# Kernel tuning notes

Measured on AMD Instinct MI355X. Metric: run time of the kernel, lower is better.

## Reference

```python
import jax, jax.numpy as jnp
import numpy as np

N = 50000          # nodes
K = 16             # neighbors per node
E = N * K          # edges
C_IN = 64
C_OUT = 64
BN_EPS = 1e-5


def _batchnorm(h, gamma, beta):
    # training-mode BatchNorm1d over the edge dimension (biased variance, as torch)
    mean = jnp.mean(h, axis=0)
    var = jnp.mean((h - mean) ** 2, axis=0)
    return gamma * (h - mean) * jax.lax.rsqrt(var + BN_EPS) + beta


def setup_inputs() -> dict:
    key = jax.random.key(0)
    ks = jax.random.split(key, 8)
    x = jax.random.normal(ks[0], (N, C_IN), dtype=jnp.float32)
    # destinations: every node has exactly K incoming edges (avoids empty segments)
    dst = jnp.repeat(jnp.arange(N, dtype=jnp.int64), K)
    src = jax.random.randint(ks[1], (E,), 0, N, dtype=jnp.int64)
    edge_index = jnp.stack([src, dst], axis=0)
    s1 = 1.0 / np.sqrt(2 * C_IN)
    s2 = 1.0 / np.sqrt(C_OUT)
    params = {
        "W1": jax.random.uniform(ks[2], (2 * C_IN, C_OUT), jnp.float32, -s1, s1),
        "b1": jnp.zeros((C_OUT,), jnp.float32),
        "g1": jnp.ones((C_OUT,), jnp.float32),
        "be1": jnp.zeros((C_OUT,), jnp.float32),
        "W2": jax.random.uniform(ks[3], (C_OUT, C_OUT), jnp.float32, -s2, s2),
        "b2": jnp.zeros((C_OUT,), jnp.float32),
        "g2": jnp.ones((C_OUT,), jnp.float32),
        "be2": jnp.zeros((C_OUT,), jnp.float32),
        "W3": jax.random.uniform(ks[4], (C_OUT, C_OUT), jnp.float32, -s2, s2),
        "b3": jnp.zeros((C_OUT,), jnp.float32),
    }
    return {"x": x, "edge_index": edge_index, **params}


def reference(x, edge_index, W1, b1, g1, be1, W2, b2, g2, be2, W3, b3):
    src, dst = edge_index[0], edge_index[1]
    x_i = x[dst]                      # [E, C_in] destination (center) features
    x_j = x[src]                      # [E, C_in] source (neighbor) features
    h = jnp.concatenate([x_i, x_j - x_i], axis=-1)   # [E, 2*C_in]
    h = jax.nn.leaky_relu(_batchnorm(h @ W1 + b1, g1, be1))
    h = jax.nn.leaky_relu(_batchnorm(h @ W2 + b2, g2, be2))
    h = h @ W3 + b3                   # [E, C_out]
    out = jax.ops.segment_max(h, dst, num_segments=N)  # scatter-max per dst node
    res = x                           # identity residual (in_channels == out_channels)
    return jax.nn.leaky_relu(out + res)
```

## Files before the change

### kernel.cpp

```cpp
#include <hip/hip_runtime.h>
#include <hip/hip_fp16.h>

#define N_NODES 50000
#define KNN     16
#define NEDGE   (N_NODES*KNN)
#define NTILE2  (NEDGE/128)
#define NWT     (N_NODES/16)
#define NB2     1024
#define SLOPE   0.01f
#define EPS     1e-5f

typedef __attribute__((ext_vector_type(8))) _Float16 f16x8;
typedef __attribute__((ext_vector_type(4))) float f32x4;

__device__ __forceinline__ unsigned short f2h(float f){
  union{_Float16 h; unsigned short u;} v; v.h = (_Float16)f; return v.u;
}
__device__ __forceinline__ unsigned short h2u(_Float16 h){
  union{_Float16 h; unsigned short u;} v; v.h = h; return v.u;
}
__device__ __forceinline__ f32x4 MFMA(f16x8 a, f16x8 b, f32x4 c){
  return __builtin_amdgcn_mfma_f32_16x16x32_f16(a, b, c, 0, 0, 0);
}
__device__ __forceinline__ float lrelu(float v){ return v>=0.f ? v : SLOPE*v; }

__global__ __launch_bounds__(256) void kInit(const float* __restrict__ W1,
    const float* __restrict__ W2, const float* __restrict__ W3,
    unsigned short* __restrict__ wf)
{
  const int idx = blockIdx.x*256 + threadIdx.x;
  const float* W; int fi; bool fold = false;
  if (idx < 1024)      { W = W1; fi = idx >> 6; fold = (idx < 512); }
  else if (idx < 1536) { W = W2; fi = (idx-1024) >> 6; }
  else                 { W = W3; fi = (idx-1536) >> 6; }
  const int l  = idx & 63;
  const int ks = fi >> 2, nf = fi & 3;
  const int k0 = ks*32 + ((l>>4)<<3);
  const int col = nf*16 + (l&15);
  unsigned short* o = wf + (size_t)idx*8;
#pragma unroll
  for (int e=0;e<8;++e){
    float v = W[(size_t)(k0+e)*64 + col];
    if (fold) v -= W[(size_t)(k0+e+64)*64 + col];
    o[e] = f2h(v);
  }
}

__global__ __launch_bounds__(256) void kUV(const float* __restrict__ x,
    const uint4* __restrict__ wf, unsigned short* __restrict__ Ub,
    unsigned short* __restrict__ Vb)
{
  const int t = threadIdx.x, w = t>>6, l = t&63, lr = l&15, lg = l>>4;
  const int wt = blockIdx.x*4 + w;
  if (wt >= NWT) return;
  f16x8 wfr[16];
#pragma unroll
  for (int f=0;f<16;++f){ union{uint4 v; f16x8 h;}q; q.v = wf[f*64 + l]; wfr[f]=q.h; }
  const int n0 = wt*16;
  const float* xr = x + (size_t)(n0+lr)*64 + lg*8;
  f16x8 a0, a1;
#pragma unroll
  for (int e=0;e<8;++e){ a0[e] = (_Float16)xr[e]; a1[e] = (_Float16)xr[32+e]; }

  f32x4 aU[4], aV[4];
#pragma unroll
  for (int nf=0;nf<4;++nf){
    aU[nf] = (f32x4){0,0,0,0};
    aU[nf] = MFMA(a0, wfr[nf],    aU[nf]);
    aU[nf] = MFMA(a1, wfr[4+nf],  aU[nf]);
    aV[nf] = (f32x4){0,0,0,0};
    aV[nf] = MFMA(a0, wfr[8+nf],  aV[nf]);
    aV[nf] = MFMA(a1, wfr[12+nf], aV[nf]);
  }
#pragma unroll
  for (int nf=0;nf<4;++nf)
#pragma unroll
    for (int r=0;r<4;++r){
      const size_t o = (size_t)(n0 + 4*lg + r)*64 + 16*nf + lr;
      Ub[o] = f2h(aU[nf][r]);
      Vb[o] = f2h(aV[nf][r]);
    }
}

#define LOADUV(U0,U1,V0,V1, nodeId, srcId)                               \
  {                                                                      \
    const unsigned short* Ur = Ub + (size_t)(nodeId)*64 + lg*8;          \
    const unsigned short* Vr = Vb + (size_t)(srcId)*64  + lg*8;          \
    U0 = *(const f16x8*)(Ur); U1 = *(const f16x8*)(Ur + 32);             \
    V0 = *(const f16x8*)(Vr); V1 = *(const f16x8*)(Vr + 32);             \
  }

#define H1COMP(h0f, h1f, U0,U1,V0,V1)                                   \
  f16x8 h0f, h1f;                                                       \
  {                                                                     \
    const f16x8 s0 = U0 + V0, s1 = U1 + V1;                             \
    h0f = __builtin_elementwise_max(s0, s0 * (_Float16)0.01f);          \
    h1f = __builtin_elementwise_max(s1, s1 * (_Float16)0.01f);          \
  }

__global__ __launch_bounds__(256,4) void kS1(const unsigned short* __restrict__ Ub,
    const unsigned short* __restrict__ Vb, const int* __restrict__ ei,
    float* __restrict__ part)
{
  __shared__ float red[4][128];
  const int t = threadIdx.x, w = t>>6, l = t&63, lr = l&15, lg = l>>4;
  const int G = gridDim.x;

  float s[16], q[16];
#pragma unroll
  for (int k=0;k<16;++k){ s[k]=0.f; q[k]=0.f; }

#define ACCST(U0,U1,V0,V1)                                              \
  {                                                                     \
    const f16x8 z0 = U0 + V0, z1 = U1 + V1;                             \
    _Pragma("unroll")                                                   \
    for (int e=0;e<8;++e){ const float zf=(float)z0[e]; s[e]+=zf; q[e]=fmaf(zf,zf,q[e]); } \
    _Pragma("unroll")                                                   \
    for (int e=0;e<8;++e){ const float zf=(float)z1[e]; s[8+e]+=zf; q[8+e]=fmaf(zf,zf,q[8+e]); } \
  }

  int tile = blockIdx.x;
  int srcA = ei[tile*128 + (2*w)*16 + lr];
  int srcB = ei[tile*128 + (2*w+1)*16 + lr];
  for (; tile < NTILE2; tile += G){
    const int nA = tile*8 + 2*w, nB = nA + 1;
    f16x8 uA0,uA1,vA0,vA1, uB0,uB1,vB0,vB1;
    LOADUV(uA0,uA1,vA0,vA1, nA, srcA)
    LOADUV(uB0,uB1,vB0,vB1, nB, srcB)
    const int nt = tile + G;
    if (nt < NTILE2){
      srcA = ei[nt*128 + (2*w)*16 + lr];
      srcB = ei[nt*128 + (2*w+1)*16 + lr];
    }
    ACCST(uA0,uA1,vA0,vA1)
    ACCST(uB0,uB1,vB0,vB1)
  }

#pragma unroll
  for (int k=0;k<16;++k){
    float a=s[k]; a+=__shfl_xor(a,1,64); a+=__shfl_xor(a,2,64);
    a+=__shfl_xor(a,4,64); a+=__shfl_xor(a,8,64); s[k]=a;
    float b=q[k]; b+=__shfl_xor(b,1,64); b+=__shfl_xor(b,2,64);
    b+=__shfl_xor(b,4,64); b+=__shfl_xor(b,8,64); q[k]=b;
  }
  if (lr == 0){
#pragma unroll
    for (int e=0;e<8;++e){
      red[w][8*lg+e]    = s[e];
      red[w][32+8*lg+e] = s[8+e];
      red[w][64+8*lg+e] = q[e];
      red[w][96+8*lg+e] = q[8+e];
    }
  }
  __syncthreads();
  if (t < 128)
    part[(size_t)t*NB2 + blockIdx.x] = red[0][t]+red[1][t]+red[2][t]+red[3][t];
}

__global__ __launch_bounds__(256) void kFin(const float* __restrict__ part,
    const float* __restrict__ g, const float* __restrict__ be,
    float* __restrict__ coefs, int nb)
{
  __shared__ float rs[256], rq[256];
  const int c = blockIdx.x, t = threadIdx.x;
  const float* ps = part + (size_t)c*nb;
  const float* pq = part + (size_t)(64+c)*nb;
  float s = 0.f, q = 0.f;
  for (int i=t; i<nb; i+=256){ s += ps[i]; q += pq[i]; }
  rs[t]=s; rq[t]=q;
  __syncthreads();
#pragma unroll
  for (int off=128; off>0; off>>=1){
    if (t < off){ rs[t]+=rs[t+off]; rq[t]+=rq[t+off]; }
    __syncthreads();
  }
  if (t==0){
    const float inv  = 1.0f/(float)NEDGE;
    const float mean = rs[0]*inv;
    const float var  = rq[0]*inv - mean*mean;
    const float a    = g[c]*rsqrtf(var + EPS);
    coefs[c]      = a;
    coefs[64 + c] = be[c] - mean*a;
  }
}

__global__ __launch_bounds__(256) void kScale(unsigned short* __restrict__ Ub,
    unsigned short* __restrict__ Vb, const float* __restrict__ coefs)
{
  const int j = blockIdx.x*256 + threadIdx.x;
  if (j >= N_NODES*8) return;
  const int c0 = (j & 7)*8;
  float a[8], c[8];
#pragma unroll
  for (int e=0;e<8;++e){ a[e]=coefs[c0+e]; c[e]=coefs[64+c0+e]; }
  f16x8 u = ((const f16x8*)Ub)[j];
#pragma unroll
  for (int e=0;e<8;++e) u[e] = (_Float16)fmaf(a[e], (float)u[e], c[e]);
  ((f16x8*)Ub)[j] = u;
  f16x8 v = ((const f16x8*)Vb)[j];
#pragma unroll
  for (int e=0;e<8;++e) v[e] = (_Float16)(a[e] * (float)v[e]);
  ((f16x8*)Vb)[j] = v;
}

__global__ __launch_bounds__(256,4) void kS2(const unsigned short* __restrict__ Ub,
    const unsigned short* __restrict__ Vb, const int* __restrict__ ei,
    const uint4* __restrict__ wfg, float* __restrict__ part)
{
  __shared__ uint4 wlds[512];
  __shared__ float red[4][128];
  const int t = threadIdx.x, w = t>>6, l = t&63, lr = l&15, lg = l>>4;
  const int G = gridDim.x;
  const f32x4 Z4 = (f32x4){0.f,0.f,0.f,0.f};

  for (int i=t; i<512; i+=256) wlds[i] = wfg[1024+i];
  __syncthreads();

  float sumP[4] = {0,0,0,0}, sqP[4] = {0,0,0,0};

  int tile = blockIdx.x;
  int srcA = ei[tile*128 + (2*w)*16 + lr];
  int srcB = ei[tile*128 + (2*w+1)*16 + lr];
  for (; tile < NTILE2; tile += G){
    const int nA = tile*8 + 2*w, nB = nA + 1;
    f16x8 uA0,uA1,vA0,vA1, uB0,uB1,vB0,vB1;
    LOADUV(uA0,uA1,vA0,vA1, nA, srcA)
    LOADUV(uB0,uB1,vB0,vB1, nB, srcB)
    const int nt = tile + G;
    if (nt < NTILE2){
      srcA = ei[nt*128 + (2*w)*16 + lr];
      srcB = ei[nt*128 + (2*w+1)*16 + lr];
    }

    H1COMP(hA0, hA1, uA0,uA1,vA0,vA1)
    H1COMP(hB0, hB1, uB0,uB1,vB0,vB1)

    f32x4 aA[4], aB[4];
#pragma unroll
    for (int nf=0;nf<4;++nf){
      union{uint4 v; f16x8 h;}q0, q1;
      q0.v = wlds[nf*64 + l];  q1.v = wlds[(4+nf)*64 + l];
      aA[nf] = MFMA(hA0, q0.h, Z4);  aA[nf] = MFMA(hA1, q1.h, aA[nf]);
      aB[nf] = MFMA(hB0, q0.h, Z4);  aB[nf] = MFMA(hB1, q1.h, aB[nf]);
    }
#pragma unroll
    for (int nf=0;nf<4;++nf)
#pragma unroll
      for (int r=0;r<4;++r){
        const float v0 = aA[nf][r], v1 = aB[nf][r];
        sumP[nf] += v0 + v1;
        sqP[nf] = fmaf(v0,v0,sqP[nf]);
        sqP[nf] = fmaf(v1,v1,sqP[nf]);
      }
  }

#pragma unroll
  for (int nf=0;nf<4;++nf){
    float s = sumP[nf], q = sqP[nf];
    s += __shfl_xor(s,16,64); s += __shfl_xor(s,32,64);
    q += __shfl_xor(q,16,64); q += __shfl_xor(q,32,64);
    if (l < 16){ red[w][nf*16+l] = s; red[w][64+nf*16+l] = q; }
  }
  __syncthreads();
  if (t < 128)
    part[(size_t)t*NB2 + blockIdx.x] = red[0][t]+red[1][t]+red[2][t]+red[3][t];
}

__global__ __launch_bounds__(256,4) void kS3(const unsigned short* __restrict__ Ub,
    const unsigned short* __restrict__ Vb, const int* __restrict__ ei,
    const uint4* __restrict__ wfg, const float* __restrict__ coefs2,
    const float* __restrict__ b3, const float* __restrict__ x,
    float* __restrict__ out)
{
  __shared__ uint4 wlds[1024];
  __shared__ __align__(16) unsigned short buf[8][16][72];
  const int t = threadIdx.x, w = t>>6, l = t&63, lr = l&15, lg = l>>4;
  const int G = gridDim.x;
  const f32x4 Z4 = (f32x4){0.f,0.f,0.f,0.f};

  for (int i=t; i<1024; i+=256) wlds[i] = wfg[1024+i];
  __syncthreads();

  float a2v[4], c2v[4], bb[4];
#pragma unroll
  for (int nf=0;nf<4;++nf){
    a2v[nf]=coefs2[nf*16+lr]; c2v[nf]=coefs2[64+nf*16+lr];
    bb[nf] = b3[nf*16+lr];
  }

  int tile = blockIdx.x;
  int srcA = ei[tile*128 + (2*w)*16 + lr];
  int srcB = ei[tile*128 + (2*w+1)*16 + lr];
  for (; tile < NTILE2; tile += G){
    const int nA = tile*8 + 2*w, nB = nA + 1;
    f16x8 uA0,uA1,vA0,vA1, uB0,uB1,vB0,vB1;
    LOADUV(uA0,uA1,vA0,vA1, nA, srcA)
    LOADUV(uB0,uB1,vB0,vB1, nB, srcB)
    const int nt = tile + G;
    if (nt < NTILE2){
      srcA = ei[nt*128 + (2*w)*16 + lr];
      srcB = ei[nt*128 + (2*w+1)*16 + lr];
    }

    H1COMP(hA0, hA1, uA0,uA1,vA0,vA1)
    H1COMP(hB0, hB1, uB0,uB1,vB0,vB1)

    f32x4 aA[4], aB[4];
#pragma unroll
    for (int nf=0;nf<4;++nf){
      union{uint4 v; f16x8 h;}q0, q1;
      q0.v = wlds[nf*64 + l];  q1.v = wlds[(4+nf)*64 + l];
      aA[nf] = MFMA(hA0, q0.h, Z4);  aA[nf] = MFMA(hA1, q1.h, aA[nf]);
      aB[nf] = MFMA(hB0, q0.h, Z4);  aB[nf] = MFMA(hB1, q1.h, aB[nf]);
    }
#pragma unroll
    for (int nf=0;nf<4;++nf)
#pragma unroll
      for (int r=0;r<4;++r){
        buf[2*w  ][4*lg+r][16*nf+lr] = h2u((_Float16)lrelu(fmaf(a2v[nf], aA[nf][r], c2v[nf])));
        buf[2*w+1][4*lg+r][16*nf+lr] = h2u((_Float16)lrelu(fmaf(a2v[nf], aB[nf][r], c2v[nf])));
      }
    const f16x8 gA0 = *(const f16x8*)&buf[2*w  ][lr][8*lg];
    const f16x8 gA1 = *(const f16x8*)&buf[2*w  ][lr][32+8*lg];
    const f16x8 gB0 = *(const f16x8*)&buf[2*w+1][lr][8*lg];
    const f16x8 gB1 = *(const f16x8*)&buf[2*w+1][lr][32+8*lg];

    f32x4 cA[4], cB[4];
#pragma unroll
    for (int nf=0;nf<4;++nf){
      union{uint4 v; f16x8 h;}q0, q1;
      q0.v = wlds[512 + nf*64 + l];  q1.v = wlds[512 + (4+nf)*64 + l];
      cA[nf] = MFMA(gA0, q0.h, Z4);  cA[nf] = MFMA(gA1, q1.h, cA[nf]);
      cB[nf] = MFMA(gB0, q0.h, Z4);  cB[nf] = MFMA(gB1, q1.h, cB[nf]);
    }

#pragma unroll
    for (int nf=0;nf<4;++nf){
      float mA = fmaxf(fmaxf(cA[nf][0],cA[nf][1]), fmaxf(cA[nf][2],cA[nf][3]));
      mA = fmaxf(mA, __shfl_xor(mA,16,64));
      mA = fmaxf(mA, __shfl_xor(mA,32,64));
      float mB = fmaxf(fmaxf(cB[nf][0],cB[nf][1]), fmaxf(cB[nf][2],cB[nf][3]));
      mB = fmaxf(mB, __shfl_xor(mB,16,64));
      mB = fmaxf(mB, __shfl_xor(mB,32,64));
      if (l < 16){
        const float xA = x[(size_t)nA*64 + nf*16 + l];
        out[(size_t)nA*64 + nf*16 + l] = lrelu(mA + bb[nf] + xA);
        const float xB = x[(size_t)nB*64 + nf*16 + l];
        out[(size_t)nB*64 + nf*16 + l] = lrelu(mB + bb[nf] + xB);
      }
    }
  }
}

extern "C" void kernel_launch(void* const* d_in, const int* in_sizes, int n_in,
                              void* d_out, int out_size, void* d_ws, size_t ws_size,
                              hipStream_t stream) {
  const float* x   = (const float*)d_in[0];
  const int*   ei  = (const int*)d_in[1];
  const float* W1  = (const float*)d_in[2];
  const float* g1  = (const float*)d_in[4];
  const float* be1 = (const float*)d_in[5];
  const float* W2  = (const float*)d_in[6];
  const float* g2  = (const float*)d_in[8];
  const float* be2 = (const float*)d_in[9];
  const float* W3  = (const float*)d_in[10];
  const float* b3  = (const float*)d_in[11];
  float* out = (float*)d_out;

  float*          coefs = (float*)d_ws;
  float*          part1 = (float*)((char*)d_ws + 1024);
  float*          part2 = part1 + (size_t)NB2*128;
  unsigned short* wfb   = (unsigned short*)((char*)part2 + (size_t)NB2*128*4);
  unsigned short* Ub    = (unsigned short*)((char*)wfb + 32768);
  unsigned short* Vb    = Ub + (size_t)N_NODES*64;

  kInit<<<8, 256, 0, stream>>>(W1, W2, W3, wfb);
  kUV<<<(NWT+3)/4, 256, 0, stream>>>(x, (const uint4*)wfb, Ub, Vb);
  kS1<<<NB2, 256, 0, stream>>>(Ub, Vb, ei, part1);
  kFin<<<64, 256, 0, stream>>>(part1, g1, be1, coefs, NB2);
  kScale<<<(N_NODES*8 + 255)/256, 256, 0, stream>>>(Ub, Vb, coefs);
  kS2<<<NB2, 256, 0, stream>>>(Ub, Vb, ei, (const uint4*)wfb, part2);
  kFin<<<64, 256, 0, stream>>>(part2, g2, be2, coefs + 128, NB2);
  kS3<<<NB2, 256, 0, stream>>>(Ub, Vb, ei, (const uint4*)wfb, coefs + 128,
                               b3, x, out);
}
```

Before: 108.4 us.

## Fuse weight prep into kUV/kS1 and apply BN1 affine inside kS2/kS3

Removes the kInit launch: kUV now builds its W1 MFMA fragments directly from fp32 W1, and the first four blocks of kS1 pack W2/W3 into the fragment buffer. Removes the kScale pass over U/V, applying the BN1 scale and shift in fp16 registers inside kS2 and kS3 instead. This saves two launches and a full read/write sweep of U and V. In exchange it adds per-edge fp16 FMA work, a different fp16 rounding order for the BN1 affine, and redundant W1 loads in every kUV wave.

Measured after the change: 107.0 us. No clear change (-1.2%).

```diff
diff --git a/kernel.cpp b/kernel.cpp
--- a/kernel.cpp
+++ b/kernel.cpp
@@ -24,38 +24,30 @@
 }
 __device__ __forceinline__ float lrelu(float v){ return v>=0.f ? v : SLOPE*v; }
 
-__global__ __launch_bounds__(256) void kInit(const float* __restrict__ W1,
-    const float* __restrict__ W2, const float* __restrict__ W3,
-    unsigned short* __restrict__ wf)
-{
-  const int idx = blockIdx.x*256 + threadIdx.x;
-  const float* W; int fi; bool fold = false;
-  if (idx < 1024)      { W = W1; fi = idx >> 6; fold = (idx < 512); }
-  else if (idx < 1536) { W = W2; fi = (idx-1024) >> 6; }
-  else                 { W = W3; fi = (idx-1536) >> 6; }
-  const int l  = idx & 63;
-  const int ks = fi >> 2, nf = fi & 3;
-  const int k0 = ks*32 + ((l>>4)<<3);
-  const int col = nf*16 + (l&15);
-  unsigned short* o = wf + (size_t)idx*8;
-#pragma unroll
-  for (int e=0;e<8;++e){
-    float v = W[(size_t)(k0+e)*64 + col];
-    if (fold) v -= W[(size_t)(k0+e+64)*64 + col];
-    o[e] = f2h(v);
-  }
-}
-
 __global__ __launch_bounds__(256) void kUV(const float* __restrict__ x,
-    const uint4* __restrict__ wf, unsigned short* __restrict__ Ub,
+    const float* __restrict__ W1, unsigned short* __restrict__ Ub,
     unsigned short* __restrict__ Vb)
 {
   const int t = threadIdx.x, w = t>>6, l = t&63, lr = l&15, lg = l>>4;
   const int wt = blockIdx.x*4 + w;
   if (wt >= NWT) return;
+
   f16x8 wfr[16];
 #pragma unroll
-  for (int f=0;f<16;++f){ union{uint4 v; f16x8 h;}q; q.v = wf[f*64 + l]; wfr[f]=q.h; }
+  for (int f=0;f<16;++f){
+    const int ks = f>>2, nf = f&3;
+    const int k0 = ks*32 + (lg<<3);
+    const int col = nf*16 + lr;
+    f16x8 r;
+#pragma unroll
+    for (int e=0;e<8;++e){
+      float v = W1[(size_t)(k0+e)*64 + col];
+      if (f < 8) v -= W1[(size_t)(k0+e+64)*64 + col];
+      r[e] = (_Float16)v;
+    }
+    wfr[f] = r;
+  }
+
   const int n0 = wt*16;
   const float* xr = x + (size_t)(n0+lr)*64 + lg*8;
   f16x8 a0, a1;
@@ -90,21 +82,27 @@
     V0 = *(const f16x8*)(Vr); V1 = *(const f16x8*)(Vr + 32);             \
   }
 
-#define H1COMP(h0f, h1f, U0,U1,V0,V1)                                   \
-  f16x8 h0f, h1f;                                                       \
-  {                                                                     \
-    const f16x8 s0 = U0 + V0, s1 = U1 + V1;                             \
-    h0f = __builtin_elementwise_max(s0, s0 * (_Float16)0.01f);          \
-    h1f = __builtin_elementwise_max(s1, s1 * (_Float16)0.01f);          \
-  }
-
 __global__ __launch_bounds__(256,4) void kS1(const unsigned short* __restrict__ Ub,
     const unsigned short* __restrict__ Vb, const int* __restrict__ ei,
-    float* __restrict__ part)
+    const float* __restrict__ W2, const float* __restrict__ W3,
+    unsigned short* __restrict__ wf, float* __restrict__ part)
 {
   __shared__ float red[4][128];
   const int t = threadIdx.x, w = t>>6, l = t&63, lr = l&15, lg = l>>4;
   const int G = gridDim.x;
+
+  if (blockIdx.x < 4){
+    const int idx = blockIdx.x*256 + t;
+    const float* W = (idx < 512) ? W2 : W3;
+    const int fi = (idx & 511) >> 6;
+    const int ll = idx & 63;
+    const int ks = fi >> 2, nf = fi & 3;
+    const int k0 = ks*32 + ((ll>>4)<<3);
+    const int col = nf*16 + (ll&15);
+    unsigned short* o = wf + (size_t)idx*8;
+#pragma unroll
+    for (int e=0;e<8;++e) o[e] = f2h(W[(size_t)(k0+e)*64 + col]);
+  }
 
   float s[16], q[16];
 #pragma unroll
@@ -184,28 +182,30 @@
   }
 }
 
-__global__ __launch_bounds__(256) void kScale(unsigned short* __restrict__ Ub,
-    unsigned short* __restrict__ Vb, const float* __restrict__ coefs)
-{
-  const int j = blockIdx.x*256 + threadIdx.x;
-  if (j >= N_NODES*8) return;
-  const int c0 = (j & 7)*8;
-  float a[8], c[8];
-#pragma unroll
-  for (int e=0;e<8;++e){ a[e]=coefs[c0+e]; c[e]=coefs[64+c0+e]; }
-  f16x8 u = ((const f16x8*)Ub)[j];
-#pragma unroll
-  for (int e=0;e<8;++e) u[e] = (_Float16)fmaf(a[e], (float)u[e], c[e]);
-  ((f16x8*)Ub)[j] = u;
-  f16x8 v = ((const f16x8*)Vb)[j];
-#pragma unroll
-  for (int e=0;e<8;++e) v[e] = (_Float16)(a[e] * (float)v[e]);
-  ((f16x8*)Vb)[j] = v;
-}
+#define LOAD_C1                                                         \
+  f16x8 A1a, A1b, C1a, C1b;                                             \
+  {                                                                     \
+    const int kb = lg*8;                                                \
+    _Pragma("unroll")                                                   \
+    for (int e=0;e<8;++e){                                              \
+      A1a[e] = (_Float16)coefs1[kb+e];    A1b[e] = (_Float16)coefs1[32+kb+e]; \
+      C1a[e] = (_Float16)coefs1[64+kb+e]; C1b[e] = (_Float16)coefs1[96+kb+e]; \
+    }                                                                   \
+  }
+
+#define H1F(h0f, h1f, U0,U1,V0,V1)                                      \
+  f16x8 h0f, h1f;                                                       \
+  {                                                                     \
+    const f16x8 t0 = (U0 + V0) * A1a + C1a;                             \
+    const f16x8 t1 = (U1 + V1) * A1b + C1b;                             \
+    h0f = __builtin_elementwise_max(t0, t0 * (_Float16)0.01f);          \
+    h1f = __builtin_elementwise_max(t1, t1 * (_Float16)0.01f);          \
+  }
 
 __global__ __launch_bounds__(256,4) void kS2(const unsigned short* __restrict__ Ub,
     const unsigned short* __restrict__ Vb, const int* __restrict__ ei,
-    const uint4* __restrict__ wfg, float* __restrict__ part)
+    const uint4* __restrict__ wfg, const float* __restrict__ coefs1,
+    float* __restrict__ part)
 {
   __shared__ uint4 wlds[512];
   __shared__ float red[4][128];
@@ -213,8 +213,9 @@
   const int G = gridDim.x;
   const f32x4 Z4 = (f32x4){0.f,0.f,0.f,0.f};
 
-  for (int i=t; i<512; i+=256) wlds[i] = wfg[1024+i];
-  __syncthreads();
+  for (int i=t; i<512; i+=256) wlds[i] = wfg[i];
+  __syncthreads();
+  LOAD_C1
 
   float sumP[4] = {0,0,0,0}, sqP[4] = {0,0,0,0};
 
@@ -232,8 +233,8 @@
       srcB = ei[nt*128 + (2*w+1)*16 + lr];
     }
 
-    H1COMP(hA0, hA1, uA0,uA1,vA0,vA1)
-    H1COMP(hB0, hB1, uB0,uB1,vB0,vB1)
+    H1F(hA0, hA1, uA0,uA1,vA0,vA1)
+    H1F(hB0, hB1, uB0,uB1,vB0,vB1)
 
     f32x4 aA[4], aB[4];
 #pragma unroll
@@ -268,9 +269,9 @@
 
 __global__ __launch_bounds__(256,4) void kS3(const unsigned short* __restrict__ Ub,
     const unsigned short* __restrict__ Vb, const int* __restrict__ ei,
-    const uint4* __restrict__ wfg, const float* __restrict__ coefs2,
-    const float* __restrict__ b3, const float* __restrict__ x,
-    float* __restrict__ out)
+    const uint4* __restrict__ wfg, const float* __restrict__ coefs1,
+    const float* __restrict__ coefs2, const float* __restrict__ b3,
+    const float* __restrict__ x, float* __restrict__ out)
 {
   __shared__ uint4 wlds[1024];
   __shared__ __align__(16) unsigned short buf[8][16][72];
@@ -278,8 +279,9 @@
   const int G = gridDim.x;
   const f32x4 Z4 = (f32x4){0.f,0.f,0.f,0.f};
 
-  for (int i=t; i<1024; i+=256) wlds[i] = wfg[1024+i];
-  __syncthreads();
+  for (int i=t; i<1024; i+=256) wlds[i] = wfg[i];
+  __syncthreads();
+  LOAD_C1
 
   float a2v[4], c2v[4], bb[4];
 #pragma unroll
@@ -302,8 +304,8 @@
       srcB = ei[nt*128 + (2*w+1)*16 + lr];
     }
 
-    H1COMP(hA0, hA1, uA0,uA1,vA0,vA1)
-    H1COMP(hB0, hB1, uB0,uB1,vB0,vB1)
+    H1F(hA0, hA1, uA0,uA1,vA0,vA1)
+    H1F(hB0, hB1, uB0,uB1,vB0,vB1)
 
     f32x4 aA[4], aB[4];
 #pragma unroll
@@ -371,16 +373,14 @@
   float*          part1 = (float*)((char*)d_ws + 1024);
   float*          part2 = part1 + (size_t)NB2*128;
   unsigned short* wfb   = (unsigned short*)((char*)part2 + (size_t)NB2*128*4);
-  unsigned short* Ub    = (unsigned short*)((char*)wfb + 32768);
+  unsigned short* Ub    = (unsigned short*)((char*)wfb + 16384);
   unsigned short* Vb    = Ub + (size_t)N_NODES*64;
 
-  kInit<<<8, 256, 0, stream>>>(W1, W2, W3, wfb);
-  kUV<<<(NWT+3)/4, 256, 0, stream>>>(x, (const uint4*)wfb, Ub, Vb);
-  kS1<<<NB2, 256, 0, stream>>>(Ub, Vb, ei, part1);
+  kUV<<<(NWT+3)/4, 256, 0, stream>>>(x, W1, Ub, Vb);
+  kS1<<<NB2, 256, 0, stream>>>(Ub, Vb, ei, W2, W3, wfb, part1);
   kFin<<<64, 256, 0, stream>>>(part1, g1, be1, coefs, NB2);
-  kScale<<<(N_NODES*8 + 255)/256, 256, 0, stream>>>(Ub, Vb, coefs);
-  kS2<<<NB2, 256, 0, stream>>>(Ub, Vb, ei, (const uint4*)wfb, part2);
+  kS2<<<NB2, 256, 0, stream>>>(Ub, Vb, ei, (const uint4*)wfb, coefs, part2);
   kFin<<<64, 256, 0, stream>>>(part2, g2, be2, coefs + 128, NB2);
-  kS3<<<NB2, 256, 0, stream>>>(Ub, Vb, ei, (const uint4*)wfb, coefs + 128,
-                               b3, x, out);
-}
+  kS3<<<NB2, 256, 0, stream>>>(Ub, Vb, ei, (const uint4*)wfb, coefs,
+                               coefs + 128, b3, x, out);
+}
```
